# Kernel tuning notes

Measured on AMD Instinct MI355X. Metric: run time of the kernel, lower is better.

The kernel has to match this reference:

```python
import jax, jax.numpy as jnp
import numpy as np

FP8_MAX = 448.0  # torch.finfo(float8_e4m3fn).max
BLK = 128
EPS = 1e-12

def fp8_round(x):
    # saturated cast to float8_e4m3fn and back (emulates to_fp8_saturated)
    y = jnp.clip(x, -FP8_MAX, FP8_MAX)
    return y.astype(jnp.float8_e4m3fn).astype(jnp.float32)

def per_tile_quant_dequant(x):
    # activation: 1x128 tiles along the feature dim
    S, D = x.shape
    t = x.reshape(S, D // BLK, BLK)
    amax = jnp.max(jnp.abs(t), axis=-1, keepdims=True)
    scale = jnp.maximum(amax, EPS) / FP8_MAX
    q = fp8_round(t / scale)
    return (q * scale).reshape(S, D)

def per_block_quant_dequant_weight(w):
    # weight: 128x128 blocks, w is [ne, dout, din]
    ne, do, di = w.shape
    blk = w.reshape(ne, do // BLK, BLK, di // BLK, BLK)
    amax = jnp.max(jnp.abs(blk), axis=(2, 4), keepdims=True)
    scale = jnp.maximum(amax, EPS) / FP8_MAX
    q = fp8_round(blk / scale)
    return (q * scale).reshape(ne, do, di)

def setup_inputs() -> dict:
    key = jax.random.key(0)
    k1, k2 = jax.random.split(key)
    NE, DOUT, DIN, SEQ = 8, 1024, 2048, 16384
    x = jax.random.normal(k1, (SEQ, DIN), dtype=jnp.float32)
    w = jax.random.normal(k2, (NE * DOUT, DIN), dtype=jnp.float32) * 0.02
    tokens_per_expert = jnp.full((NE,), SEQ // NE, dtype=jnp.int32)
    return {"input": x, "tokens_per_expert": tokens_per_expert, "weight": w}

def reference(input, tokens_per_expert, weight):
    NE = tokens_per_expert.shape[0]
    S, DIN = input.shape
    DOUT = weight.shape[0] // NE
    w = weight.reshape(NE, DOUT, DIN)
    w_dq = per_block_quant_dequant_weight(w)   # fp8 per-block weight, dequantized
    x_dq = per_tile_quant_dequant(input)       # fp8 per-tile activation, dequantized
    # grouped varlen GEMM; tokens are split equally across experts here
    T = S // NE
    xe = x_dq.reshape(NE, T, DIN)
    out = jnp.einsum('etd,eod->eto', xe, w_dq)  # [ne, T, dout]
    return out.reshape(S, DOUT)
```

## Files before the change

### kernel.cpp

```cpp
#include <hip/hip_runtime.h>
#include <hip/hip_bf16.h>
#include <hip/hip_fp8.h>

#define SEQ   16384
#define DIN_  2048
#define DOUT_ 1024
#define NE_   8
#define TPE   (SEQ / NE_)
#define NT    (DIN_ / 64)

typedef __bf16 bf16x8 __attribute__((ext_vector_type(8)));
typedef __bf16 bf16x4 __attribute__((ext_vector_type(4)));
typedef float  f32x4  __attribute__((ext_vector_type(4)));

#define GLD(gp, lp) __builtin_amdgcn_global_load_lds( \
    (const __attribute__((address_space(1))) unsigned int*)(gp), \
    (__attribute__((address_space(3))) unsigned int*)(lp), 16, 0, 0)

__device__ __forceinline__ float fp8_round_dq_m(float v, float sinv, float s) {
    float r = v * sinv;
    r = fminf(fmaxf(r, -448.0f), 448.0f);
    __hip_fp8_e4m3 q(r);
    return (float)q * s;
}

__global__ __launch_bounds__(256) void quant_kernel(const float* __restrict__ X,
                                                    const float* __restrict__ W,
                                                    __bf16* __restrict__ Xq,
                                                    __bf16* __restrict__ Wq) {
    const int t = threadIdx.x;
    if (blockIdx.x < SEQ) {
        const int row  = blockIdx.x;
        const int lane = t & 63;
        const int wave = t >> 6;
        const int tile = wave * 4 + (lane >> 4);
        const int sub  = lane & 15;

        const float* p = X + (size_t)row * DIN_ + tile * 128 + sub * 8;
        float4 v0 = *(const float4*)p;
        float4 v1 = *(const float4*)(p + 4);

        float m = fmaxf(fmaxf(fmaxf(fabsf(v0.x), fabsf(v0.y)), fmaxf(fabsf(v0.z), fabsf(v0.w))),
                        fmaxf(fmaxf(fabsf(v1.x), fabsf(v1.y)), fmaxf(fabsf(v1.z), fabsf(v1.w))));
        #pragma unroll
        for (int off = 1; off < 16; off <<= 1)
            m = fmaxf(m, __shfl_xor(m, off, 64));

        const float s    = fmaxf(m, 1e-12f) / 448.0f;
        const float sinv = 1.0f / s;

        bf16x8 o;
        o[0] = (__bf16)fp8_round_dq_m(v0.x, sinv, s);
        o[1] = (__bf16)fp8_round_dq_m(v0.y, sinv, s);
        o[2] = (__bf16)fp8_round_dq_m(v0.z, sinv, s);
        o[3] = (__bf16)fp8_round_dq_m(v0.w, sinv, s);
        o[4] = (__bf16)fp8_round_dq_m(v1.x, sinv, s);
        o[5] = (__bf16)fp8_round_dq_m(v1.y, sinv, s);
        o[6] = (__bf16)fp8_round_dq_m(v1.z, sinv, s);
        o[7] = (__bf16)fp8_round_dq_m(v1.w, sinv, s);
        *(bf16x8*)(Xq + (size_t)row * DIN_ + tile * 128 + sub * 8) = o;
    } else {
        const int b  = blockIdx.x - SEQ;
        const int rb = b >> 4;
        const int cb = b & 15;

        const float* base = W + (size_t)(rb * 128) * DIN_ + cb * 128;
        const int r0 = t >> 5;
        const int c0 = (t & 31) * 4;

        float4 v[16];
        float m = 0.0f;
        #pragma unroll
        for (int i = 0; i < 16; ++i) {
            v[i] = *(const float4*)(base + (size_t)(i * 8 + r0) * DIN_ + c0);
            m = fmaxf(m, fmaxf(fmaxf(fabsf(v[i].x), fabsf(v[i].y)),
                               fmaxf(fabsf(v[i].z), fabsf(v[i].w))));
        }
        #pragma unroll
        for (int off = 1; off < 64; off <<= 1)
            m = fmaxf(m, __shfl_xor(m, off, 64));
        __shared__ float smx[4];
        if ((t & 63) == 0) smx[t >> 6] = m;
        __syncthreads();
        const float amax = fmaxf(fmaxf(smx[0], smx[1]), fmaxf(smx[2], smx[3]));
        const float s    = fmaxf(amax, 1e-12f) / 448.0f;
        const float sinv = 1.0f / s;

        __bf16* obase = Wq + (size_t)(rb * 128) * DIN_ + cb * 128;
        #pragma unroll
        for (int i = 0; i < 16; ++i) {
            bf16x4 o;
            o[0] = (__bf16)fp8_round_dq_m(v[i].x, sinv, s);
            o[1] = (__bf16)fp8_round_dq_m(v[i].y, sinv, s);
            o[2] = (__bf16)fp8_round_dq_m(v[i].z, sinv, s);
            o[3] = (__bf16)fp8_round_dq_m(v[i].w, sinv, s);
            *(bf16x4*)(obase + (size_t)(i * 8 + r0) * DIN_ + c0) = o;
        }
    }
}

__global__ __launch_bounds__(512, 2) void gemm_kernel(const __bf16* __restrict__ X,
                                                      const __bf16* __restrict__ W,
                                                      float* __restrict__ out) {
    __shared__ __bf16 lds[65536];

    const int bid  = blockIdx.x;
    const int wgid = (bid & 7) * 32 + (bid >> 3);
    const int e    = wgid >> 5;
    const int tile = wgid & 31;
    const int brow = tile >> 2;
    const int bcol = tile & 3;

    const int t     = threadIdx.x;
    const int lane  = t & 63;
    const int wave  = t >> 6;
    const int wm    = wave >> 2;
    const int wn    = wave & 3;
    const int flane = lane & 15;

    const __bf16* Xt = X + (size_t)(e * TPE + brow * 256) * DIN_;
    const __bf16* Wt = W + (size_t)(e * DOUT_ + bcol * 256) * DIN_;

    auto stage_half = [&](int H) {
        if (H >= 4 * NT) return;
        const int kt2  = H >> 2;
        const int typ  = H & 3;
        const int kh   = typ >> 1;
        const bool isA = (typ & 1) != 0;
        const int buf  = kt2 & 1;
        const __bf16* src = isA ? Xt : Wt;
        const unsigned rbase = (isA ? 0u : 32768u) + (unsigned)(buf * 2 + kh) * 8192u;
        #pragma unroll
        for (int i = 0; i < 2; ++i) {
            const unsigned p = (unsigned)i * 8192u + (unsigned)t * 16u;
            const unsigned q = p ^ (((p >> 7) & 3u) << 4);
            const unsigned srow = q >> 6;
            const unsigned scol = (q & 63u) >> 1;
            GLD(src + (size_t)srow * DIN_ + kt2 * 64 + kh * 32 + scol,
                &lds[rbase + p / 2]);
        }
    };

    auto ld_frag = [&](unsigned rbase, int row) -> bf16x8 {
        unsigned p = (unsigned)row * 64u + (unsigned)(lane >> 4) * 16u;
        p ^= ((p >> 7) & 3u) << 4;
        return *(const bf16x8*)&lds[rbase + p / 2];
    };

    f32x4 acc[8][4] = {};

    stage_half(0); stage_half(1); stage_half(2); stage_half(3);
    stage_half(4); stage_half(5); stage_half(6);
    asm volatile("s_waitcnt vmcnt(6)" ::: "memory");
    __builtin_amdgcn_s_barrier();

    for (int kt = 0; kt < NT; ++kt) {
        const int buf = kt & 1;
        const unsigned A0 = (unsigned)(buf * 2 + 0) * 8192u;
        const unsigned A1 = (unsigned)(buf * 2 + 1) * 8192u;
        const unsigned B0 = 32768u + (unsigned)(buf * 2 + 0) * 8192u;
        const unsigned B1 = 32768u + (unsigned)(buf * 2 + 1) * 8192u;
        const int H0 = 4 * kt + 7;

        bf16x8 a[4], b[4];

        #pragma unroll
        for (int n = 0; n < 4; ++n) b[n] = ld_frag(B0, wn * 64 + n * 16 + flane);
        #pragma unroll
        for (int m = 0; m < 4; ++m) a[m] = ld_frag(A0, wm * 128 + m * 16 + flane);
        stage_half(H0);
        __builtin_amdgcn_s_barrier();
        asm volatile("s_waitcnt lgkmcnt(0)" ::: "memory");
        __builtin_amdgcn_sched_barrier(0);
        __builtin_amdgcn_s_setprio(1);
        #pragma unroll
        for (int m = 0; m < 4; ++m)
            #pragma unroll
            for (int n = 0; n < 4; ++n)
                acc[m][n] = __builtin_amdgcn_mfma_f32_16x16x32_bf16(a[m], b[n], acc[m][n], 0, 0, 0);
        __builtin_amdgcn_s_setprio(0);
        __builtin_amdgcn_s_barrier();

        #pragma unroll
        for (int m = 0; m < 4; ++m) a[m] = ld_frag(A0, wm * 128 + (m + 4) * 16 + flane);
        stage_half(H0 + 1);
        __builtin_amdgcn_s_barrier();
        asm volatile("s_waitcnt lgkmcnt(0)" ::: "memory");
        __builtin_amdgcn_sched_barrier(0);
        __builtin_amdgcn_s_setprio(1);
        #pragma unroll
        for (int m = 0; m < 4; ++m)
            #pragma unroll
            for (int n = 0; n < 4; ++n)
                acc[m + 4][n] = __builtin_amdgcn_mfma_f32_16x16x32_bf16(a[m], b[n], acc[m + 4][n], 0, 0, 0);
        __builtin_amdgcn_s_setprio(0);
        __builtin_amdgcn_s_barrier();

        #pragma unroll
        for (int n = 0; n < 4; ++n) b[n] = ld_frag(B1, wn * 64 + n * 16 + flane);
        #pragma unroll
        for (int m = 0; m < 4; ++m) a[m] = ld_frag(A1, wm * 128 + m * 16 + flane);
        stage_half(H0 + 2);
        __builtin_amdgcn_s_barrier();
        asm volatile("s_waitcnt lgkmcnt(0)" ::: "memory");
        __builtin_amdgcn_sched_barrier(0);
        __builtin_amdgcn_s_setprio(1);
        #pragma unroll
        for (int m = 0; m < 4; ++m)
            #pragma unroll
            for (int n = 0; n < 4; ++n)
                acc[m][n] = __builtin_amdgcn_mfma_f32_16x16x32_bf16(a[m], b[n], acc[m][n], 0, 0, 0);
        __builtin_amdgcn_s_setprio(0);
        __builtin_amdgcn_s_barrier();

        #pragma unroll
        for (int m = 0; m < 4; ++m) a[m] = ld_frag(A1, wm * 128 + (m + 4) * 16 + flane);
        stage_half(H0 + 3);
        __builtin_amdgcn_s_barrier();
        asm volatile("s_waitcnt lgkmcnt(0)" ::: "memory");
        __builtin_amdgcn_sched_barrier(0);
        __builtin_amdgcn_s_setprio(1);
        #pragma unroll
        for (int m = 0; m < 4; ++m)
            #pragma unroll
            for (int n = 0; n < 4; ++n)
                acc[m + 4][n] = __builtin_amdgcn_mfma_f32_16x16x32_bf16(a[m], b[n], acc[m + 4][n], 0, 0, 0);
        __builtin_amdgcn_s_setprio(0);
        if (kt < NT - 2) {
            asm volatile("s_waitcnt vmcnt(6)" ::: "memory");
        } else {
            asm volatile("s_waitcnt vmcnt(0)" ::: "memory");
        }
        __builtin_amdgcn_s_barrier();
    }

    const int orow0 = e * TPE + brow * 256 + wm * 128;
    const int ocol0 = bcol * 256 + wn * 64;
    const int rl = (lane >> 4) * 4;
    const int cl = lane & 15;
    #pragma unroll
    for (int m = 0; m < 8; ++m)
        #pragma unroll
        for (int n = 0; n < 4; ++n)
            #pragma unroll
            for (int j = 0; j < 4; ++j) {
                const int r = orow0 + m * 16 + rl + j;
                const int c = ocol0 + n * 16 + cl;
                out[(size_t)r * DOUT_ + c] = acc[m][n][j];
            }
}

extern "C" void kernel_launch(void* const* d_in, const int* in_sizes, int n_in,
                              void* d_out, int out_size, void* d_ws, size_t ws_size,
                              hipStream_t stream) {
    const float* x = (const float*)d_in[0];
    const float* w = (const float*)d_in[2];
    float* out = (float*)d_out;

    __bf16* xq = (__bf16*)d_ws;
    __bf16* wq = (__bf16*)((char*)d_ws + (size_t)SEQ * DIN_ * sizeof(__bf16));

    quant_kernel<<<SEQ + (NE_ * DOUT_ / 128) * (DIN_ / 128), 256, 0, stream>>>(x, w, xq, wq);
    gemm_kernel<<<NE_ * (TPE / 256) * (DOUT_ / 256), 512, 0, stream>>>(xq, wq, out);
}
```

Measured before the change: 125.0 us.

## Restructure GEMM LDS layout to full-k rows and reuse B fragments; split quant kernels

The GEMM now stores each 64-wide k slice as contiguous 128-byte rows with an 8-way XOR swizzle, and stages row halves instead of k halves. The inner loop loads B fragments for both k halves once and reuses them across both M sub-tiles, which cuts LDS reads. The quantization is split into separate activation and weight kernels, with the activation kernel processing two rows per block. The aim is fewer LDS transactions and bank conflicts, at the cost of more live registers and one extra kernel launch.

```diff
diff --git a/kernel.cpp b/kernel.cpp
--- a/kernel.cpp
+++ b/kernel.cpp
@@ -24,85 +24,102 @@
     return (float)q * s;
 }
 
-__global__ __launch_bounds__(256) void quant_kernel(const float* __restrict__ X,
-                                                    const float* __restrict__ W,
-                                                    __bf16* __restrict__ Xq,
-                                                    __bf16* __restrict__ Wq) {
-    const int t = threadIdx.x;
-    if (blockIdx.x < SEQ) {
-        const int row  = blockIdx.x;
-        const int lane = t & 63;
-        const int wave = t >> 6;
-        const int tile = wave * 4 + (lane >> 4);
-        const int sub  = lane & 15;
-
-        const float* p = X + (size_t)row * DIN_ + tile * 128 + sub * 8;
-        float4 v0 = *(const float4*)p;
-        float4 v1 = *(const float4*)(p + 4);
-
-        float m = fmaxf(fmaxf(fmaxf(fabsf(v0.x), fabsf(v0.y)), fmaxf(fabsf(v0.z), fabsf(v0.w))),
-                        fmaxf(fmaxf(fabsf(v1.x), fabsf(v1.y)), fmaxf(fabsf(v1.z), fabsf(v1.w))));
-        #pragma unroll
-        for (int off = 1; off < 16; off <<= 1)
-            m = fmaxf(m, __shfl_xor(m, off, 64));
-
-        const float s    = fmaxf(m, 1e-12f) / 448.0f;
-        const float sinv = 1.0f / s;
-
-        bf16x8 o;
-        o[0] = (__bf16)fp8_round_dq_m(v0.x, sinv, s);
-        o[1] = (__bf16)fp8_round_dq_m(v0.y, sinv, s);
-        o[2] = (__bf16)fp8_round_dq_m(v0.z, sinv, s);
-        o[3] = (__bf16)fp8_round_dq_m(v0.w, sinv, s);
-        o[4] = (__bf16)fp8_round_dq_m(v1.x, sinv, s);
-        o[5] = (__bf16)fp8_round_dq_m(v1.y, sinv, s);
-        o[6] = (__bf16)fp8_round_dq_m(v1.z, sinv, s);
-        o[7] = (__bf16)fp8_round_dq_m(v1.w, sinv, s);
-        *(bf16x8*)(Xq + (size_t)row * DIN_ + tile * 128 + sub * 8) = o;
-    } else {
-        const int b  = blockIdx.x - SEQ;
-        const int rb = b >> 4;
-        const int cb = b & 15;
-
-        const float* base = W + (size_t)(rb * 128) * DIN_ + cb * 128;
-        const int r0 = t >> 5;
-        const int c0 = (t & 31) * 4;
-
-        float4 v[16];
-        float m = 0.0f;
-        #pragma unroll
-        for (int i = 0; i < 16; ++i) {
-            v[i] = *(const float4*)(base + (size_t)(i * 8 + r0) * DIN_ + c0);
-            m = fmaxf(m, fmaxf(fmaxf(fabsf(v[i].x), fabsf(v[i].y)),
-                               fmaxf(fabsf(v[i].z), fabsf(v[i].w))));
-        }
-        #pragma unroll
-        for (int off = 1; off < 64; off <<= 1)
-            m = fmaxf(m, __shfl_xor(m, off, 64));
-        __shared__ float smx[4];
-        if ((t & 63) == 0) smx[t >> 6] = m;
-        __syncthreads();
-        const float amax = fmaxf(fmaxf(smx[0], smx[1]), fmaxf(smx[2], smx[3]));
-        const float s    = fmaxf(amax, 1e-12f) / 448.0f;
-        const float sinv = 1.0f / s;
-
-        __bf16* obase = Wq + (size_t)(rb * 128) * DIN_ + cb * 128;
-        #pragma unroll
-        for (int i = 0; i < 16; ++i) {
-            bf16x4 o;
-            o[0] = (__bf16)fp8_round_dq_m(v[i].x, sinv, s);
-            o[1] = (__bf16)fp8_round_dq_m(v[i].y, sinv, s);
-            o[2] = (__bf16)fp8_round_dq_m(v[i].z, sinv, s);
-            o[3] = (__bf16)fp8_round_dq_m(v[i].w, sinv, s);
-            *(bf16x4*)(obase + (size_t)(i * 8 + r0) * DIN_ + c0) = o;
-        }
+__global__ __launch_bounds__(256) void quant_x_kernel(const float* __restrict__ X,
+                                                      __bf16* __restrict__ Xq) {
+    const int t    = threadIdx.x;
+    const int lane = t & 63;
+    const int wave = t >> 6;
+    const int tile = wave * 4 + (lane >> 4);
+    const int sub  = lane & 15;
+    const size_t off = (size_t)tile * 128 + sub * 8;
+
+    const int row0 = blockIdx.x * 2;
+    const float* pa = X + (size_t)row0 * DIN_ + off;
+    const float* pb = X + (size_t)(row0 + 1) * DIN_ + off;
+
+    float4 a0 = *(const float4*)pa;
+    float4 a1 = *(const float4*)(pa + 4);
+    float4 b0 = *(const float4*)pb;
+    float4 b1 = *(const float4*)(pb + 4);
+
+    float ma = fmaxf(fmaxf(fmaxf(fabsf(a0.x), fabsf(a0.y)), fmaxf(fabsf(a0.z), fabsf(a0.w))),
+                     fmaxf(fmaxf(fabsf(a1.x), fabsf(a1.y)), fmaxf(fabsf(a1.z), fabsf(a1.w))));
+    float mb = fmaxf(fmaxf(fmaxf(fabsf(b0.x), fabsf(b0.y)), fmaxf(fabsf(b0.z), fabsf(b0.w))),
+                     fmaxf(fmaxf(fabsf(b1.x), fabsf(b1.y)), fmaxf(fabsf(b1.z), fabsf(b1.w))));
+    #pragma unroll
+    for (int off2 = 1; off2 < 16; off2 <<= 1) {
+        ma = fmaxf(ma, __shfl_xor(ma, off2, 64));
+        mb = fmaxf(mb, __shfl_xor(mb, off2, 64));
+    }
+
+    const float sa = fmaxf(ma, 1e-12f) / 448.0f, sia = 1.0f / sa;
+    const float sb = fmaxf(mb, 1e-12f) / 448.0f, sib = 1.0f / sb;
+
+    bf16x8 oa, ob;
+    oa[0] = (__bf16)fp8_round_dq_m(a0.x, sia, sa);
+    oa[1] = (__bf16)fp8_round_dq_m(a0.y, sia, sa);
+    oa[2] = (__bf16)fp8_round_dq_m(a0.z, sia, sa);
+    oa[3] = (__bf16)fp8_round_dq_m(a0.w, sia, sa);
+    oa[4] = (__bf16)fp8_round_dq_m(a1.x, sia, sa);
+    oa[5] = (__bf16)fp8_round_dq_m(a1.y, sia, sa);
+    oa[6] = (__bf16)fp8_round_dq_m(a1.z, sia, sa);
+    oa[7] = (__bf16)fp8_round_dq_m(a1.w, sia, sa);
+    ob[0] = (__bf16)fp8_round_dq_m(b0.x, sib, sb);
+    ob[1] = (__bf16)fp8_round_dq_m(b0.y, sib, sb);
+    ob[2] = (__bf16)fp8_round_dq_m(b0.z, sib, sb);
+    ob[3] = (__bf16)fp8_round_dq_m(b0.w, sib, sb);
+    ob[4] = (__bf16)fp8_round_dq_m(b1.x, sib, sb);
+    ob[5] = (__bf16)fp8_round_dq_m(b1.y, sib, sb);
+    ob[6] = (__bf16)fp8_round_dq_m(b1.z, sib, sb);
+    ob[7] = (__bf16)fp8_round_dq_m(b1.w, sib, sb);
+    *(bf16x8*)(Xq + (size_t)row0 * DIN_ + off) = oa;
+    *(bf16x8*)(Xq + (size_t)(row0 + 1) * DIN_ + off) = ob;
+}
+
+__global__ __launch_bounds__(256) void quant_w_kernel(const float* __restrict__ W,
+                                                      __bf16* __restrict__ Wq) {
+    const int rb = blockIdx.x >> 4;
+    const int cb = blockIdx.x & 15;
+    const int t  = threadIdx.x;
+
+    const float* base = W + (size_t)(rb * 128) * DIN_ + cb * 128;
+    const int r0 = t >> 5;
+    const int c0 = (t & 31) * 4;
+
+    float4 v[16];
+    float m = 0.0f;
+    #pragma unroll
+    for (int i = 0; i < 16; ++i) {
+        v[i] = *(const float4*)(base + (size_t)(i * 8 + r0) * DIN_ + c0);
+        m = fmaxf(m, fmaxf(fmaxf(fabsf(v[i].x), fabsf(v[i].y)),
+                           fmaxf(fabsf(v[i].z), fabsf(v[i].w))));
+    }
+    #pragma unroll
+    for (int off = 1; off < 64; off <<= 1)
+        m = fmaxf(m, __shfl_xor(m, off, 64));
+    __shared__ float smx[4];
+    if ((t & 63) == 0) smx[t >> 6] = m;
+    __syncthreads();
+    const float amax = fmaxf(fmaxf(smx[0], smx[1]), fmaxf(smx[2], smx[3]));
+    const float s    = fmaxf(amax, 1e-12f) / 448.0f;
+    const float sinv = 1.0f / s;
+
+    __bf16* obase = Wq + (size_t)(rb * 128) * DIN_ + cb * 128;
+    #pragma unroll
+    for (int i = 0; i < 16; ++i) {
+        bf16x4 o;
+        o[0] = (__bf16)fp8_round_dq_m(v[i].x, sinv, s);
+        o[1] = (__bf16)fp8_round_dq_m(v[i].y, sinv, s);
+        o[2] = (__bf16)fp8_round_dq_m(v[i].z, sinv, s);
+        o[3] = (__bf16)fp8_round_dq_m(v[i].w, sinv, s);
+        *(bf16x4*)(obase + (size_t)(i * 8 + r0) * DIN_ + c0) = o;
     }
 }
 
 __global__ __launch_bounds__(512, 2) void gemm_kernel(const __bf16* __restrict__ X,
                                                       const __bf16* __restrict__ W,
                                                       float* __restrict__ out) {
-    __shared__ __bf16 lds[65536];
+    __shared__ __align__(16) unsigned char lds[131072];
 
     const int bid  = blockIdx.x;
     const int wgid = (bid & 7) * 32 + (bid >> 3);
@@ -121,110 +138,107 @@
     const __bf16* Xt = X + (size_t)(e * TPE + brow * 256) * DIN_;
     const __bf16* Wt = W + (size_t)(e * DOUT_ + bcol * 256) * DIN_;
 
-    auto stage_half = [&](int H) {
+    auto stage_part = [&](int H) {
         if (H >= 4 * NT) return;
-        const int kt2  = H >> 2;
-        const int typ  = H & 3;
-        const int kh   = typ >> 1;
-        const bool isA = (typ & 1) != 0;
-        const int buf  = kt2 & 1;
-        const __bf16* src = isA ? Xt : Wt;
-        const unsigned rbase = (isA ? 0u : 32768u) + (unsigned)(buf * 2 + kh) * 8192u;
+        const int k2   = H >> 2;
+        const int r    = H & 3;
+        const bool isB = (r < 2);
+        const int half = r & 1;
+        const int buf  = k2 & 1;
+        const __bf16* src = isB ? Wt : Xt;
+        const unsigned base = (isB ? 65536u : 0u) + (unsigned)buf * 32768u
+                            + (unsigned)half * 16384u;
         #pragma unroll
         for (int i = 0; i < 2; ++i) {
             const unsigned p = (unsigned)i * 8192u + (unsigned)t * 16u;
-            const unsigned q = p ^ (((p >> 7) & 3u) << 4);
-            const unsigned srow = q >> 6;
-            const unsigned scol = (q & 63u) >> 1;
-            GLD(src + (size_t)srow * DIN_ + kt2 * 64 + kh * 32 + scol,
-                &lds[rbase + p / 2]);
+            const unsigned q = p ^ (((p >> 7) & 7u) << 4);
+            GLD(src + (size_t)(half * 128 + (q >> 7)) * DIN_ + k2 * 64 + ((q & 127u) >> 1),
+                &lds[base + p]);
         }
     };
 
-    auto ld_frag = [&](unsigned rbase, int row) -> bf16x8 {
-        unsigned p = (unsigned)row * 64u + (unsigned)(lane >> 4) * 16u;
-        p ^= ((p >> 7) & 3u) << 4;
-        return *(const bf16x8*)&lds[rbase + p / 2];
+    auto ld_frag = [&](unsigned base, int row, int kh) -> bf16x8 {
+        unsigned p = (unsigned)row * 128u + (unsigned)kh * 64u + (unsigned)(lane >> 4) * 16u;
+        p ^= ((p >> 7) & 7u) << 4;
+        return *(const bf16x8*)&lds[base + p];
     };
 
     f32x4 acc[8][4] = {};
 
-    stage_half(0); stage_half(1); stage_half(2); stage_half(3);
-    stage_half(4); stage_half(5); stage_half(6);
+    stage_part(0); stage_part(1); stage_part(2); stage_part(3);
+    stage_part(4); stage_part(5); stage_part(6);
     asm volatile("s_waitcnt vmcnt(6)" ::: "memory");
     __builtin_amdgcn_s_barrier();
 
     for (int kt = 0; kt < NT; ++kt) {
         const int buf = kt & 1;
-        const unsigned A0 = (unsigned)(buf * 2 + 0) * 8192u;
-        const unsigned A1 = (unsigned)(buf * 2 + 1) * 8192u;
-        const unsigned B0 = 32768u + (unsigned)(buf * 2 + 0) * 8192u;
-        const unsigned B1 = 32768u + (unsigned)(buf * 2 + 1) * 8192u;
+        const unsigned Ab = (unsigned)buf * 32768u;
+        const unsigned Bb = 65536u + (unsigned)buf * 32768u;
         const int H0 = 4 * kt + 7;
 
-        bf16x8 a[4], b[4];
-
-        #pragma unroll
-        for (int n = 0; n < 4; ++n) b[n] = ld_frag(B0, wn * 64 + n * 16 + flane);
-        #pragma unroll
-        for (int m = 0; m < 4; ++m) a[m] = ld_frag(A0, wm * 128 + m * 16 + flane);
-        stage_half(H0);
-        __builtin_amdgcn_s_barrier();
-        asm volatile("s_waitcnt lgkmcnt(0)" ::: "memory");
-        __builtin_amdgcn_sched_barrier(0);
-        __builtin_amdgcn_s_setprio(1);
-        #pragma unroll
-        for (int m = 0; m < 4; ++m)
-            #pragma unroll
-            for (int n = 0; n < 4; ++n)
-                acc[m][n] = __builtin_amdgcn_mfma_f32_16x16x32_bf16(a[m], b[n], acc[m][n], 0, 0, 0);
-        __builtin_amdgcn_s_setprio(0);
-        __builtin_amdgcn_s_barrier();
-
-        #pragma unroll
-        for (int m = 0; m < 4; ++m) a[m] = ld_frag(A0, wm * 128 + (m + 4) * 16 + flane);
-        stage_half(H0 + 1);
-        __builtin_amdgcn_s_barrier();
-        asm volatile("s_waitcnt lgkmcnt(0)" ::: "memory");
-        __builtin_amdgcn_sched_barrier(0);
-        __builtin_amdgcn_s_setprio(1);
-        #pragma unroll
-        for (int m = 0; m < 4; ++m)
-            #pragma unroll
-            for (int n = 0; n < 4; ++n)
-                acc[m + 4][n] = __builtin_amdgcn_mfma_f32_16x16x32_bf16(a[m], b[n], acc[m + 4][n], 0, 0, 0);
-        __builtin_amdgcn_s_setprio(0);
-        __builtin_amdgcn_s_barrier();
-
-        #pragma unroll
-        for (int n = 0; n < 4; ++n) b[n] = ld_frag(B1, wn * 64 + n * 16 + flane);
-        #pragma unroll
-        for (int m = 0; m < 4; ++m) a[m] = ld_frag(A1, wm * 128 + m * 16 + flane);
-        stage_half(H0 + 2);
-        __builtin_amdgcn_s_barrier();
-        asm volatile("s_waitcnt lgkmcnt(0)" ::: "memory");
-        __builtin_amdgcn_sched_barrier(0);
-        __builtin_amdgcn_s_setprio(1);
-        #pragma unroll
-        for (int m = 0; m < 4; ++m)
-            #pragma unroll
-            for (int n = 0; n < 4; ++n)
-                acc[m][n] = __builtin_amdgcn_mfma_f32_16x16x32_bf16(a[m], b[n], acc[m][n], 0, 0, 0);
-        __builtin_amdgcn_s_setprio(0);
-        __builtin_amdgcn_s_barrier();
-
-        #pragma unroll
-        for (int m = 0; m < 4; ++m) a[m] = ld_frag(A1, wm * 128 + (m + 4) * 16 + flane);
-        stage_half(H0 + 3);
-        __builtin_amdgcn_s_barrier();
-        asm volatile("s_waitcnt lgkmcnt(0)" ::: "memory");
-        __builtin_amdgcn_sched_barrier(0);
-        __builtin_amdgcn_s_setprio(1);
-        #pragma unroll
-        for (int m = 0; m < 4; ++m)
-            #pragma unroll
-            for (int n = 0; n < 4; ++n)
-                acc[m + 4][n] = __builtin_amdgcn_mfma_f32_16x16x32_bf16(a[m], b[n], acc[m + 4][n], 0, 0, 0);
+        bf16x8 b0[4], b1[4], a[4];
+
+        #pragma unroll
+        for (int n = 0; n < 4; ++n) b0[n] = ld_frag(Bb, wn * 64 + n * 16 + flane, 0);
+        #pragma unroll
+        for (int m = 0; m < 4; ++m) a[m] = ld_frag(Ab, wm * 128 + m * 16 + flane, 0);
+        stage_part(H0);
+        __builtin_amdgcn_s_barrier();
+        asm volatile("s_waitcnt lgkmcnt(0)" ::: "memory");
+        __builtin_amdgcn_sched_barrier(0);
+        __builtin_amdgcn_s_setprio(1);
+        #pragma unroll
+        for (int m = 0; m < 4; ++m)
+            #pragma unroll
+            for (int n = 0; n < 4; ++n)
+                acc[m][n] = __builtin_amdgcn_mfma_f32_16x16x32_bf16(a[m], b0[n], acc[m][n], 0, 0, 0);
+        __builtin_amdgcn_s_setprio(0);
+        __builtin_amdgcn_s_barrier();
+
+        #pragma unroll
+        for (int n = 0; n < 4; ++n) b1[n] = ld_frag(Bb, wn * 64 + n * 16 + flane, 1);
+        #pragma unroll
+        for (int m = 0; m < 4; ++m) a[m] = ld_frag(Ab, wm * 128 + m * 16 + flane, 1);
+        stage_part(H0 + 1);
+        __builtin_amdgcn_s_barrier();
+        asm volatile("s_waitcnt lgkmcnt(0)" ::: "memory");
+        __builtin_amdgcn_sched_barrier(0);
+        __builtin_amdgcn_s_setprio(1);
+        #pragma unroll
+        for (int m = 0; m < 4; ++m)
+            #pragma unroll
+            for (int n = 0; n < 4; ++n)
+                acc[m][n] = __builtin_amdgcn_mfma_f32_16x16x32_bf16(a[m], b1[n], acc[m][n], 0, 0, 0);
+        __builtin_amdgcn_s_setprio(0);
+        __builtin_amdgcn_s_barrier();
+
+        #pragma unroll
+        for (int m = 0; m < 4; ++m) a[m] = ld_frag(Ab, wm * 128 + (m + 4) * 16 + flane, 0);
+        stage_part(H0 + 2);
+        __builtin_amdgcn_s_barrier();
+        asm volatile("s_waitcnt lgkmcnt(0)" ::: "memory");
+        __builtin_amdgcn_sched_barrier(0);
+        __builtin_amdgcn_s_setprio(1);
+        #pragma unroll
+        for (int m = 0; m < 4; ++m)
+            #pragma unroll
+            for (int n = 0; n < 4; ++n)
+                acc[m + 4][n] = __builtin_amdgcn_mfma_f32_16x16x32_bf16(a[m], b0[n], acc[m + 4][n], 0, 0, 0);
+        __builtin_amdgcn_s_setprio(0);
+        __builtin_amdgcn_s_barrier();
+
+        #pragma unroll
+        for (int m = 0; m < 4; ++m) a[m] = ld_frag(Ab, wm * 128 + (m + 4) * 16 + flane, 1);
+        stage_part(H0 + 3);
+        __builtin_amdgcn_s_barrier();
+        asm volatile("s_waitcnt lgkmcnt(0)" ::: "memory");
+        __builtin_amdgcn_sched_barrier(0);
+        __builtin_amdgcn_s_setprio(1);
+        #pragma unroll
+        for (int m = 0; m < 4; ++m)
+            #pragma unroll
+            for (int n = 0; n < 4; ++n)
+                acc[m + 4][n] = __builtin_amdgcn_mfma_f32_16x16x32_bf16(a[m], b1[n], acc[m + 4][n], 0, 0, 0);
         __builtin_amdgcn_s_setprio(0);
         if (kt < NT - 2) {
             asm volatile("s_waitcnt vmcnt(6)" ::: "memory");
@@ -260,6 +274,7 @@
     __bf16* xq = (__bf16*)d_ws;
     __bf16* wq = (__bf16*)((char*)d_ws + (size_t)SEQ * DIN_ * sizeof(__bf16));
 
-    quant_kernel<<<SEQ + (NE_ * DOUT_ / 128) * (DIN_ / 128), 256, 0, stream>>>(x, w, xq, wq);
+    quant_x_kernel<<<SEQ / 2, 256, 0, stream>>>(x, xq);
+    quant_w_kernel<<<(NE_ * DOUT_ / 128) * (DIN_ / 128), 256, 0, stream>>>(w, wq);
     gemm_kernel<<<NE_ * (TPE / 256) * (DOUT_ / 256), 512, 0, stream>>>(xq, wq, out);
 }
```

After: 121.1 us. 1.03x faster.
